# Kernel optimization log

Measured on AMD Instinct MI355X. Metric: run time of the kernel, lower is better.

## Reference

```python
import jax, jax.numpy as jnp
import numpy as np

B, C, L = 16, 512, 4096
G = 32
CPG = C // G          # 16
HALF = CPG // 2       # 8
EPS = 1e-5


def setup_inputs() -> dict:
    key = jax.random.key(0)
    k = jax.random.split(key, 5)
    return {
        "x": jax.random.normal(k[0], (B, C, L), dtype=jnp.float32),
        "cw_w": jax.random.normal(k[1], (G,), dtype=jnp.float32),
        "cw_b": jax.random.normal(k[2], (G,), dtype=jnp.float32),
        "sw_w": jax.random.normal(k[3], (G,), dtype=jnp.float32),
        "sw_b": jax.random.normal(k[4], (G,), dtype=jnp.float32),
        "gn_w": jnp.ones((G, HALF), dtype=jnp.float32),
        "gn_b": jnp.zeros((G, HALF), dtype=jnp.float32),
    }


def reference(x, cw_w, cw_b, sw_w, sw_b, gn_w, gn_b):
    b, c, l = x.shape
    g = cw_w.shape[0]
    cpg = c // g
    half = cpg // 2
    xg = x.reshape(b, g, cpg, l)
    x1 = xg[:, :, :half, :]   # [B,G,half,L] channel-attention half
    x2 = xg[:, :, half:, :]   # [B,G,half,L] spatial-attention half

    # channel attention: per-channel temporal mean -> scalar affine + sigmoid
    ca = x1.mean(axis=3)                                          # [B,G,half]
    w1 = jax.nn.sigmoid(ca * cw_w[None, :, None] + cw_b[None, :, None])
    x1e = x1 * w1[..., None]

    # GroupNorm(1, half): normalize over (channels, length) per (sample, group)
    mu = x2.mean(axis=(2, 3), keepdims=True)
    var = x2.var(axis=(2, 3), keepdims=True)                      # biased var, as in torch GroupNorm
    xn = (x2 - mu) * jax.lax.rsqrt(var + EPS)
    xn = xn * gn_w[None, :, :, None] + gn_b[None, :, :, None]

    # spatial attention: channel-mean of normalized -> scalar affine + sigmoid
    sm = xn.mean(axis=2)                                          # [B,G,L]
    w2 = jax.nn.sigmoid(sm * sw_w[None, :, None] + sw_b[None, :, None])
    x2e = x2 * w2[:, :, None, :]

    out = jnp.concatenate([x1e, x2e], axis=2)                     # [B,G,cpg,L]
    # final channel shuffle: view->transpose(1,2)->view
    out = out.transpose(0, 2, 1, 3).reshape(b, c, l)
    return out
```

## Files before the change

kernel.cpp:

```cpp
#include <hip/hip_runtime.h>
#include <math.h>

#define Bdim 16
#define Cdim 512
#define Ldim 4096
#define Gdim 32
#define CPG  16
#define HALF 8
#define EPSV 1e-5f

#define THREADS 512
#define NWAVES  (THREADS / 64)

__device__ __forceinline__ float wave_reduce_sum(float v) {
#pragma unroll
    for (int off = 32; off > 0; off >>= 1)
        v += __shfl_xor(v, off, 64);
    return v;
}

__device__ __forceinline__ float sigmoidf_(float x) {
    return 1.0f / (1.0f + expf(-x));
}

__global__ __launch_bounds__(THREADS, 4) void fused_ham_kernel(
    const float* __restrict__ x,
    const float* __restrict__ cw_w, const float* __restrict__ cw_b,
    const float* __restrict__ sw_w, const float* __restrict__ sw_b,
    const float* __restrict__ gn_w, const float* __restrict__ gn_b,
    float* __restrict__ out)
{
    const int bg   = blockIdx.x;
    const int b    = bg / Gdim;
    const int g    = bg % Gdim;
    const int tid  = threadIdx.x;
    const int wave = tid >> 6;
    const int lane = tid & 63;

    __shared__ float red1[NWAVES][HALF];
    __shared__ float red2[NWAVES][2];

    const float* xb   = x + ((size_t)b * Cdim + (size_t)g * CPG) * Ldim;
    float*       outb = out + (size_t)b * Cdim * Ldim;

    const int l0 = tid * 4;

    float4 a[HALF][2];
    float  s1[HALF];
#pragma unroll
    for (int c = 0; c < HALF; ++c) {
        s1[c] = 0.f;
#pragma unroll
        for (int j = 0; j < 2; ++j) {
            const float4 v = *reinterpret_cast<const float4*>(
                xb + (size_t)c * Ldim + j * (Ldim / 2) + l0);
            a[c][j] = v;
            s1[c] += (v.x + v.y) + (v.z + v.w);
        }
    }
#pragma unroll
    for (int c = 0; c < HALF; ++c) {
        const float t = wave_reduce_sum(s1[c]);
        if (lane == 0) red1[wave][c] = t;
    }
    __syncthreads();

    float w1[HALF];
    {
        const float cww = cw_w[g], cwb = cw_b[g];
#pragma unroll
        for (int c = 0; c < HALF; ++c) {
            float s = 0.f;
#pragma unroll
            for (int w = 0; w < NWAVES; ++w) s += red1[w][c];
            const float ca = s * (1.0f / Ldim);
            w1[c] = sigmoidf_(ca * cww + cwb);
        }
    }

#pragma unroll
    for (int c = 0; c < HALF; ++c) {
        float* o = outb + (size_t)(c * Gdim + g) * Ldim;
#pragma unroll
        for (int j = 0; j < 2; ++j) {
            float4 v = a[c][j];
            v.x *= w1[c]; v.y *= w1[c]; v.z *= w1[c]; v.w *= w1[c];
            *reinterpret_cast<float4*>(o + j * (Ldim / 2) + l0) = v;
        }
    }

    float4 bb[HALF][2];
    float  sum = 0.f, ssq = 0.f;
#pragma unroll
    for (int c = 0; c < HALF; ++c) {
#pragma unroll
        for (int j = 0; j < 2; ++j) {
            const float4 v = *reinterpret_cast<const float4*>(
                xb + (size_t)(HALF + c) * Ldim + j * (Ldim / 2) + l0);
            bb[c][j] = v;
            sum += (v.x + v.y) + (v.z + v.w);
            ssq += (v.x * v.x + v.y * v.y) + (v.z * v.z + v.w * v.w);
        }
    }
    sum = wave_reduce_sum(sum);
    ssq = wave_reduce_sum(ssq);
    if (lane == 0) { red2[wave][0] = sum; red2[wave][1] = ssq; }
    __syncthreads();

    float tsum = 0.f, tssq = 0.f;
#pragma unroll
    for (int w = 0; w < NWAVES; ++w) { tsum += red2[w][0]; tssq += red2[w][1]; }
    const float inv_n = 1.0f / (HALF * Ldim);
    const float mu    = tsum * inv_n;
    const float var   = tssq * inv_n - mu * mu;
    const float rs    = rsqrtf(var + EPSV);

    float gw[HALF];
    float sgw = 0.f, mgb = 0.f;
#pragma unroll
    for (int c = 0; c < HALF; ++c) {
        gw[c] = gn_w[g * HALF + c];
        sgw  += gw[c];
        mgb  += gn_b[g * HALF + c];
    }
    mgb *= (1.0f / HALF);
    const float sww = sw_w[g], swb = sw_b[g];

#pragma unroll
    for (int j = 0; j < 2; ++j) {
        float4 ws; ws.x = 0.f; ws.y = 0.f; ws.z = 0.f; ws.w = 0.f;
#pragma unroll
        for (int c = 0; c < HALF; ++c) {
            ws.x += gw[c] * bb[c][j].x;
            ws.y += gw[c] * bb[c][j].y;
            ws.z += gw[c] * bb[c][j].z;
            ws.w += gw[c] * bb[c][j].w;
        }
        const float k0 = rs * (1.0f / HALF);
        const float koff = -mu * sgw;
        float4 w2;
        w2.x = sigmoidf_(((ws.x + koff) * k0 + mgb) * sww + swb);
        w2.y = sigmoidf_(((ws.y + koff) * k0 + mgb) * sww + swb);
        w2.z = sigmoidf_(((ws.z + koff) * k0 + mgb) * sww + swb);
        w2.w = sigmoidf_(((ws.w + koff) * k0 + mgb) * sww + swb);

#pragma unroll
        for (int c = 0; c < HALF; ++c) {
            float* o = outb + (size_t)((HALF + c) * Gdim + g) * Ldim;
            float4 v = bb[c][j];
            v.x *= w2.x; v.y *= w2.y; v.z *= w2.z; v.w *= w2.w;
            *reinterpret_cast<float4*>(o + j * (Ldim / 2) + l0) = v;
        }
    }
}

extern "C" void kernel_launch(void* const* d_in, const int* in_sizes, int n_in,
                              void* d_out, int out_size, void* d_ws, size_t ws_size,
                              hipStream_t stream) {
    const float* x    = (const float*)d_in[0];
    const float* cw_w = (const float*)d_in[1];
    const float* cw_b = (const float*)d_in[2];
    const float* sw_w = (const float*)d_in[3];
    const float* sw_b = (const float*)d_in[4];
    const float* gn_w = (const float*)d_in[5];
    const float* gn_b = (const float*)d_in[6];
    float* out = (float*)d_out;

    fused_ham_kernel<<<dim3(Bdim * Gdim), dim3(THREADS), 0, stream>>>(
        x, cw_w, cw_b, sw_w, sw_b, gn_w, gn_b, out);
}
```

Before: 53.68 us.

## Split fused kernel into stats, finalize, and apply passes over L-slices

Replaces the single fused kernel, which ran one block per (batch, group) and held the whole group in registers, with three kernels. The first computes partial statistics over quarter-length slices, the second combines them into per-group coefficients, and the third re-reads x to apply the attention weights. This spreads the work over four times as many smaller blocks to raise occupancy and parallelism. The cost is a second full read of x from memory and two extra kernel launches.

```diff
diff --git a/kernel.cpp b/kernel.cpp
--- a/kernel.cpp
+++ b/kernel.cpp
@@ -9,8 +9,15 @@
 #define HALF 8
 #define EPSV 1e-5f
 
-#define THREADS 512
+#define THREADS 256
 #define NWAVES  (THREADS / 64)
+#define QSPLIT  4
+#define NBG     (Bdim * Gdim)
+#define NBLK    (NBG * QSPLIT)
+#define LSLICE  (Ldim / QSPLIT)
+
+#define WS_PART_STRIDE 10
+#define WS_STATS_OFF   (NBG * QSPLIT * WS_PART_STRIDE)
 
 __device__ __forceinline__ float wave_reduce_sum(float v) {
 #pragma unroll
@@ -23,134 +30,155 @@
     return 1.0f / (1.0f + expf(-x));
 }
 
-__global__ __launch_bounds__(THREADS, 4) void fused_ham_kernel(
-    const float* __restrict__ x,
+__global__ __launch_bounds__(THREADS, 8) void k1_stats(
+    const float* __restrict__ x, float* __restrict__ ws)
+{
+    const int bid = blockIdx.x;
+    const int bg  = bid >> 2;
+    const int q   = bid & 3;
+    const int b   = bg >> 5;
+    const int g   = bg & 31;
+    const int tid = threadIdx.x;
+    const int wave = tid >> 6;
+    const int lane = tid & 63;
+
+    const float* xb = x + ((size_t)b * Cdim + (size_t)g * CPG) * Ldim
+                        + q * LSLICE + tid * 4;
+
+    float acc[10];
+#pragma unroll
+    for (int k = 0; k < 10; ++k) acc[k] = 0.f;
+
+#pragma unroll
+    for (int c = 0; c < HALF; ++c) {
+        const float4 v = *reinterpret_cast<const float4*>(xb + (size_t)c * Ldim);
+        acc[c] = (v.x + v.y) + (v.z + v.w);
+    }
+#pragma unroll
+    for (int c = 0; c < HALF; ++c) {
+        const float4 v = *reinterpret_cast<const float4*>(xb + (size_t)(HALF + c) * Ldim);
+        acc[8] += (v.x + v.y) + (v.z + v.w);
+        acc[9] += (v.x * v.x + v.y * v.y) + (v.z * v.z + v.w * v.w);
+    }
+
+    __shared__ float red[NWAVES][10];
+#pragma unroll
+    for (int k = 0; k < 10; ++k) {
+        const float t = wave_reduce_sum(acc[k]);
+        if (lane == 0) red[wave][k] = t;
+    }
+    __syncthreads();
+
+    if (tid < 10) {
+        float s = 0.f;
+#pragma unroll
+        for (int w = 0; w < NWAVES; ++w) s += red[w][tid];
+        ws[(size_t)bid * WS_PART_STRIDE + tid] = s;
+    }
+}
+
+__global__ __launch_bounds__(THREADS) void k2_finalize(
+    const float* __restrict__ ws_in, float* __restrict__ ws_out,
     const float* __restrict__ cw_w, const float* __restrict__ cw_b,
     const float* __restrict__ sw_w, const float* __restrict__ sw_b,
-    const float* __restrict__ gn_w, const float* __restrict__ gn_b,
-    float* __restrict__ out)
+    const float* __restrict__ gn_w, const float* __restrict__ gn_b)
 {
-    const int bg   = blockIdx.x;
-    const int b    = bg / Gdim;
-    const int g    = bg % Gdim;
-    const int tid  = threadIdx.x;
-    const int wave = tid >> 6;
-    const int lane = tid & 63;
-
-    __shared__ float red1[NWAVES][HALF];
-    __shared__ float red2[NWAVES][2];
-
-    const float* xb   = x + ((size_t)b * Cdim + (size_t)g * CPG) * Ldim;
-    float*       outb = out + (size_t)b * Cdim * Ldim;
-
-    const int l0 = tid * 4;
-
-    float4 a[HALF][2];
-    float  s1[HALF];
-#pragma unroll
-    for (int c = 0; c < HALF; ++c) {
-        s1[c] = 0.f;
-#pragma unroll
-        for (int j = 0; j < 2; ++j) {
-            const float4 v = *reinterpret_cast<const float4*>(
-                xb + (size_t)c * Ldim + j * (Ldim / 2) + l0);
-            a[c][j] = v;
-            s1[c] += (v.x + v.y) + (v.z + v.w);
-        }
-    }
-#pragma unroll
-    for (int c = 0; c < HALF; ++c) {
-        const float t = wave_reduce_sum(s1[c]);
-        if (lane == 0) red1[wave][c] = t;
-    }
-    __syncthreads();
-
-    float w1[HALF];
-    {
-        const float cww = cw_w[g], cwb = cw_b[g];
-#pragma unroll
-        for (int c = 0; c < HALF; ++c) {
-            float s = 0.f;
-#pragma unroll
-            for (int w = 0; w < NWAVES; ++w) s += red1[w][c];
-            const float ca = s * (1.0f / Ldim);
-            w1[c] = sigmoidf_(ca * cww + cwb);
-        }
-    }
-
-#pragma unroll
-    for (int c = 0; c < HALF; ++c) {
-        float* o = outb + (size_t)(c * Gdim + g) * Ldim;
-#pragma unroll
-        for (int j = 0; j < 2; ++j) {
-            float4 v = a[c][j];
-            v.x *= w1[c]; v.y *= w1[c]; v.z *= w1[c]; v.w *= w1[c];
-            *reinterpret_cast<float4*>(o + j * (Ldim / 2) + l0) = v;
-        }
-    }
-
-    float4 bb[HALF][2];
-    float  sum = 0.f, ssq = 0.f;
-#pragma unroll
-    for (int c = 0; c < HALF; ++c) {
-#pragma unroll
-        for (int j = 0; j < 2; ++j) {
-            const float4 v = *reinterpret_cast<const float4*>(
-                xb + (size_t)(HALF + c) * Ldim + j * (Ldim / 2) + l0);
-            bb[c][j] = v;
-            sum += (v.x + v.y) + (v.z + v.w);
-            ssq += (v.x * v.x + v.y * v.y) + (v.z * v.z + v.w * v.w);
-        }
-    }
-    sum = wave_reduce_sum(sum);
-    ssq = wave_reduce_sum(ssq);
-    if (lane == 0) { red2[wave][0] = sum; red2[wave][1] = ssq; }
-    __syncthreads();
-
-    float tsum = 0.f, tssq = 0.f;
-#pragma unroll
-    for (int w = 0; w < NWAVES; ++w) { tsum += red2[w][0]; tssq += red2[w][1]; }
+    const int bg = blockIdx.x * THREADS + threadIdx.x;
+    if (bg >= NBG) return;
+    const int g = bg & 31;
+
+    float s[10];
+#pragma unroll
+    for (int k = 0; k < 10; ++k) {
+        float t = 0.f;
+#pragma unroll
+        for (int q = 0; q < QSPLIT; ++q)
+            t += ws_in[((size_t)bg * QSPLIT + q) * WS_PART_STRIDE + k];
+        s[k] = t;
+    }
+
+    const float cww = cw_w[g], cwb = cw_b[g];
+    float* o = ws_out + (size_t)bg * 10;
+#pragma unroll
+    for (int c = 0; c < HALF; ++c) {
+        const float ca = s[c] * (1.0f / Ldim);
+        o[c] = sigmoidf_(ca * cww + cwb);
+    }
+
     const float inv_n = 1.0f / (HALF * Ldim);
-    const float mu    = tsum * inv_n;
-    const float var   = tssq * inv_n - mu * mu;
-    const float rs    = rsqrtf(var + EPSV);
-
-    float gw[HALF];
+    const float mu  = s[8] * inv_n;
+    const float var = s[9] * inv_n - mu * mu;
+    const float rs  = rsqrtf(var + EPSV);
+
     float sgw = 0.f, mgb = 0.f;
 #pragma unroll
     for (int c = 0; c < HALF; ++c) {
-        gw[c] = gn_w[g * HALF + c];
-        sgw  += gw[c];
-        mgb  += gn_b[g * HALF + c];
+        sgw += gn_w[g * HALF + c];
+        mgb += gn_b[g * HALF + c];
     }
     mgb *= (1.0f / HALF);
+
     const float sww = sw_w[g], swb = sw_b[g];
-
-#pragma unroll
-    for (int j = 0; j < 2; ++j) {
-        float4 ws; ws.x = 0.f; ws.y = 0.f; ws.z = 0.f; ws.w = 0.f;
-#pragma unroll
-        for (int c = 0; c < HALF; ++c) {
-            ws.x += gw[c] * bb[c][j].x;
-            ws.y += gw[c] * bb[c][j].y;
-            ws.z += gw[c] * bb[c][j].z;
-            ws.w += gw[c] * bb[c][j].w;
-        }
-        const float k0 = rs * (1.0f / HALF);
-        const float koff = -mu * sgw;
-        float4 w2;
-        w2.x = sigmoidf_(((ws.x + koff) * k0 + mgb) * sww + swb);
-        w2.y = sigmoidf_(((ws.y + koff) * k0 + mgb) * sww + swb);
-        w2.z = sigmoidf_(((ws.z + koff) * k0 + mgb) * sww + swb);
-        w2.w = sigmoidf_(((ws.w + koff) * k0 + mgb) * sww + swb);
-
-#pragma unroll
-        for (int c = 0; c < HALF; ++c) {
-            float* o = outb + (size_t)((HALF + c) * Gdim + g) * Ldim;
-            float4 v = bb[c][j];
-            v.x *= w2.x; v.y *= w2.y; v.z *= w2.z; v.w *= w2.w;
-            *reinterpret_cast<float4*>(o + j * (Ldim / 2) + l0) = v;
-        }
+    const float k0  = rs * (1.0f / HALF);
+    o[8] = k0 * sww;
+    o[9] = (-mu * sgw * k0 + mgb) * sww + swb;
+}
+
+__global__ __launch_bounds__(THREADS, 8) void k3_apply(
+    const float* __restrict__ x, const float* __restrict__ stats,
+    const float* __restrict__ gn_w, float* __restrict__ out)
+{
+    const int bid = blockIdx.x;
+    const int bg  = bid >> 2;
+    const int q   = bid & 3;
+    const int b   = bg >> 5;
+    const int g   = bg & 31;
+    const int tid = threadIdx.x;
+
+    const size_t loff = (size_t)(q * LSLICE + tid * 4);
+    const float* xb   = x + ((size_t)b * Cdim + (size_t)g * CPG) * Ldim + loff;
+    float*       outb = out + (size_t)b * Cdim * Ldim + loff;
+
+    const float* st = stats + (size_t)bg * 10;
+    const float A2 = st[8], B2 = st[9];
+
+    float4 a[HALF];
+#pragma unroll
+    for (int c = 0; c < HALF; ++c)
+        a[c] = *reinterpret_cast<const float4*>(xb + (size_t)c * Ldim);
+#pragma unroll
+    for (int c = 0; c < HALF; ++c) {
+        const float w1 = st[c];
+        float4 v = a[c];
+        v.x *= w1; v.y *= w1; v.z *= w1; v.w *= w1;
+        *reinterpret_cast<float4*>(outb + (size_t)(c * Gdim + g) * Ldim) = v;
+    }
+
+    float4 bb[HALF];
+#pragma unroll
+    for (int c = 0; c < HALF; ++c)
+        bb[c] = *reinterpret_cast<const float4*>(xb + (size_t)(HALF + c) * Ldim);
+
+    float4 wsum; wsum.x = 0.f; wsum.y = 0.f; wsum.z = 0.f; wsum.w = 0.f;
+#pragma unroll
+    for (int c = 0; c < HALF; ++c) {
+        const float gw = gn_w[g * HALF + c];
+        wsum.x += gw * bb[c].x;
+        wsum.y += gw * bb[c].y;
+        wsum.z += gw * bb[c].z;
+        wsum.w += gw * bb[c].w;
+    }
+    float4 w2;
+    w2.x = sigmoidf_(A2 * wsum.x + B2);
+    w2.y = sigmoidf_(A2 * wsum.y + B2);
+    w2.z = sigmoidf_(A2 * wsum.z + B2);
+    w2.w = sigmoidf_(A2 * wsum.w + B2);
+
+#pragma unroll
+    for (int c = 0; c < HALF; ++c) {
+        float4 v = bb[c];
+        v.x *= w2.x; v.y *= w2.y; v.z *= w2.z; v.w *= w2.w;
+        *reinterpret_cast<float4*>(outb + (size_t)((HALF + c) * Gdim + g) * Ldim) = v;
     }
 }
 
@@ -165,7 +193,13 @@
     const float* gn_w = (const float*)d_in[5];
     const float* gn_b = (const float*)d_in[6];
     float* out = (float*)d_out;
-
-    fused_ham_kernel<<<dim3(Bdim * Gdim), dim3(THREADS), 0, stream>>>(
-        x, cw_w, cw_b, sw_w, sw_b, gn_w, gn_b, out);
-}
+    float* ws  = (float*)d_ws;
+
+    float* ws_part  = ws;
+    float* ws_stats = ws + WS_STATS_OFF;
+
+    k1_stats<<<dim3(NBLK), dim3(THREADS), 0, stream>>>(x, ws_part);
+    k2_finalize<<<dim3((NBG + THREADS - 1) / THREADS), dim3(THREADS), 0, stream>>>(
+        ws_part, ws_stats, cw_w, cw_b, sw_w, sw_b, gn_w, gn_b);
+    k3_apply<<<dim3(NBLK), dim3(THREADS), 0, stream>>>(x, ws_stats, gn_w, out);
+}
```

New measurement: 72.46 us. 1.35x slower.

## Split channel and spatial halves into separate blocks, re-read inputs instead of holding registers

Applied to the files above, without the earlier changes.

Launches twice as many blocks: one set handles the channel-attention half with one wave per channel row and no block-level sync, the other handles the GroupNorm/spatial half. Inputs are re-read from global memory (expected to hit cache) instead of being held in large register arrays, which lowers register pressure and allows the higher occupancy target in launch bounds. The spatial affine and sigmoid constants are folded into a single multiply-add. The cost is extra global or cache reads of x for the second pass.

```diff
diff --git a/kernel.cpp b/kernel.cpp
--- a/kernel.cpp
+++ b/kernel.cpp
@@ -11,6 +11,7 @@
 
 #define THREADS 512
 #define NWAVES  (THREADS / 64)
+#define NBG     (Bdim * Gdim)
 
 __device__ __forceinline__ float wave_reduce_sum(float v) {
 #pragma unroll
@@ -23,133 +24,110 @@
     return 1.0f / (1.0f + expf(-x));
 }
 
-__global__ __launch_bounds__(THREADS, 4) void fused_ham_kernel(
+__global__ __launch_bounds__(THREADS, 8) void fused_ham_kernel(
     const float* __restrict__ x,
     const float* __restrict__ cw_w, const float* __restrict__ cw_b,
     const float* __restrict__ sw_w, const float* __restrict__ sw_b,
     const float* __restrict__ gn_w, const float* __restrict__ gn_b,
     float* __restrict__ out)
 {
-    const int bg   = blockIdx.x;
-    const int b    = bg / Gdim;
-    const int g    = bg % Gdim;
+    const int bid  = blockIdx.x;
+    const int ph   = bid >> 9;
+    const int bg   = bid & (NBG - 1);
+    const int b    = bg >> 5;
+    const int g    = bg & 31;
     const int tid  = threadIdx.x;
     const int wave = tid >> 6;
     const int lane = tid & 63;
 
-    __shared__ float red1[NWAVES][HALF];
-    __shared__ float red2[NWAVES][2];
-
     const float* xb   = x + ((size_t)b * Cdim + (size_t)g * CPG) * Ldim;
     float*       outb = out + (size_t)b * Cdim * Ldim;
 
-    const int l0 = tid * 4;
+    if (ph == 0) {
+        const float* row = xb + (size_t)wave * Ldim;
+        float s = 0.f;
+#pragma unroll
+        for (int k = 0; k < 16; ++k) {
+            const float4 v = *reinterpret_cast<const float4*>(row + k * 256 + lane * 4);
+            s += (v.x + v.y) + (v.z + v.w);
+        }
+        s = wave_reduce_sum(s);
+        const float ca = s * (1.0f / Ldim);
+        const float w1 = sigmoidf_(ca * cw_w[g] + cw_b[g]);
 
-    float4 a[HALF][2];
-    float  s1[HALF];
+        float* orow = outb + (size_t)(wave * Gdim + g) * Ldim;
 #pragma unroll
-    for (int c = 0; c < HALF; ++c) {
-        s1[c] = 0.f;
+        for (int k = 0; k < 16; ++k) {
+            float4 v = *reinterpret_cast<const float4*>(row + k * 256 + lane * 4);
+            v.x *= w1; v.y *= w1; v.z *= w1; v.w *= w1;
+            *reinterpret_cast<float4*>(orow + k * 256 + lane * 4) = v;
+        }
+    } else {
+        const float* row = xb + (size_t)(HALF + wave) * Ldim;
+        float sum = 0.f, ssq = 0.f;
 #pragma unroll
-        for (int j = 0; j < 2; ++j) {
-            const float4 v = *reinterpret_cast<const float4*>(
-                xb + (size_t)c * Ldim + j * (Ldim / 2) + l0);
-            a[c][j] = v;
-            s1[c] += (v.x + v.y) + (v.z + v.w);
-        }
-    }
-#pragma unroll
-    for (int c = 0; c < HALF; ++c) {
-        const float t = wave_reduce_sum(s1[c]);
-        if (lane == 0) red1[wave][c] = t;
-    }
-    __syncthreads();
-
-    float w1[HALF];
-    {
-        const float cww = cw_w[g], cwb = cw_b[g];
-#pragma unroll
-        for (int c = 0; c < HALF; ++c) {
-            float s = 0.f;
-#pragma unroll
-            for (int w = 0; w < NWAVES; ++w) s += red1[w][c];
-            const float ca = s * (1.0f / Ldim);
-            w1[c] = sigmoidf_(ca * cww + cwb);
-        }
-    }
-
-#pragma unroll
-    for (int c = 0; c < HALF; ++c) {
-        float* o = outb + (size_t)(c * Gdim + g) * Ldim;
-#pragma unroll
-        for (int j = 0; j < 2; ++j) {
-            float4 v = a[c][j];
-            v.x *= w1[c]; v.y *= w1[c]; v.z *= w1[c]; v.w *= w1[c];
-            *reinterpret_cast<float4*>(o + j * (Ldim / 2) + l0) = v;
-        }
-    }
-
-    float4 bb[HALF][2];
-    float  sum = 0.f, ssq = 0.f;
-#pragma unroll
-    for (int c = 0; c < HALF; ++c) {
-#pragma unroll
-        for (int j = 0; j < 2; ++j) {
-            const float4 v = *reinterpret_cast<const float4*>(
-                xb + (size_t)(HALF + c) * Ldim + j * (Ldim / 2) + l0);
-            bb[c][j] = v;
+        for (int k = 0; k < 16; ++k) {
+            const float4 v = *reinterpret_cast<const float4*>(row + k * 256 + lane * 4);
             sum += (v.x + v.y) + (v.z + v.w);
             ssq += (v.x * v.x + v.y * v.y) + (v.z * v.z + v.w * v.w);
         }
-    }
-    sum = wave_reduce_sum(sum);
-    ssq = wave_reduce_sum(ssq);
-    if (lane == 0) { red2[wave][0] = sum; red2[wave][1] = ssq; }
-    __syncthreads();
+        sum = wave_reduce_sum(sum);
+        ssq = wave_reduce_sum(ssq);
 
-    float tsum = 0.f, tssq = 0.f;
+        __shared__ float red[NWAVES][2];
+        if (lane == 0) { red[wave][0] = sum; red[wave][1] = ssq; }
+        __syncthreads();
+
+        float tsum = 0.f, tssq = 0.f;
 #pragma unroll
-    for (int w = 0; w < NWAVES; ++w) { tsum += red2[w][0]; tssq += red2[w][1]; }
-    const float inv_n = 1.0f / (HALF * Ldim);
-    const float mu    = tsum * inv_n;
-    const float var   = tssq * inv_n - mu * mu;
-    const float rs    = rsqrtf(var + EPSV);
+        for (int w = 0; w < NWAVES; ++w) { tsum += red[w][0]; tssq += red[w][1]; }
+        const float inv_n = 1.0f / (HALF * Ldim);
+        const float mu  = tsum * inv_n;
+        const float var = tssq * inv_n - mu * mu;
+        const float rs  = rsqrtf(var + EPSV);
 
-    float gw[HALF];
-    float sgw = 0.f, mgb = 0.f;
+        float gw[HALF];
+        float sgw = 0.f, mgb = 0.f;
 #pragma unroll
-    for (int c = 0; c < HALF; ++c) {
-        gw[c] = gn_w[g * HALF + c];
-        sgw  += gw[c];
-        mgb  += gn_b[g * HALF + c];
-    }
-    mgb *= (1.0f / HALF);
-    const float sww = sw_w[g], swb = sw_b[g];
+        for (int c = 0; c < HALF; ++c) {
+            gw[c] = gn_w[g * HALF + c];
+            sgw  += gw[c];
+            mgb  += gn_b[g * HALF + c];
+        }
+        mgb *= (1.0f / HALF);
+        const float k0 = rs * (1.0f / HALF);
+        const float A2 = k0 * sw_w[g];
+        const float B2 = (-mu * sgw * k0 + mgb) * sw_w[g] + sw_b[g];
+
+        const float* xb2 = xb + (size_t)HALF * Ldim;
+#pragma unroll
+        for (int j = 0; j < 2; ++j) {
+            const int l0 = tid * 4 + j * (Ldim / 2);
+            float4 bb[HALF];
+#pragma unroll
+            for (int c = 0; c < HALF; ++c)
+                bb[c] = *reinterpret_cast<const float4*>(xb2 + (size_t)c * Ldim + l0);
+
+            float4 wsum; wsum.x = 0.f; wsum.y = 0.f; wsum.z = 0.f; wsum.w = 0.f;
+#pragma unroll
+            for (int c = 0; c < HALF; ++c) {
+                wsum.x += gw[c] * bb[c].x;
+                wsum.y += gw[c] * bb[c].y;
+                wsum.z += gw[c] * bb[c].z;
+                wsum.w += gw[c] * bb[c].w;
+            }
+            float4 w2;
+            w2.x = sigmoidf_(A2 * wsum.x + B2);
+            w2.y = sigmoidf_(A2 * wsum.y + B2);
+            w2.z = sigmoidf_(A2 * wsum.z + B2);
+            w2.w = sigmoidf_(A2 * wsum.w + B2);
 
 #pragma unroll
-    for (int j = 0; j < 2; ++j) {
-        float4 ws; ws.x = 0.f; ws.y = 0.f; ws.z = 0.f; ws.w = 0.f;
-#pragma unroll
-        for (int c = 0; c < HALF; ++c) {
-            ws.x += gw[c] * bb[c][j].x;
-            ws.y += gw[c] * bb[c][j].y;
-            ws.z += gw[c] * bb[c][j].z;
-            ws.w += gw[c] * bb[c][j].w;
-        }
-        const float k0 = rs * (1.0f / HALF);
-        const float koff = -mu * sgw;
-        float4 w2;
-        w2.x = sigmoidf_(((ws.x + koff) * k0 + mgb) * sww + swb);
-        w2.y = sigmoidf_(((ws.y + koff) * k0 + mgb) * sww + swb);
-        w2.z = sigmoidf_(((ws.z + koff) * k0 + mgb) * sww + swb);
-        w2.w = sigmoidf_(((ws.w + koff) * k0 + mgb) * sww + swb);
-
-#pragma unroll
-        for (int c = 0; c < HALF; ++c) {
-            float* o = outb + (size_t)((HALF + c) * Gdim + g) * Ldim;
-            float4 v = bb[c][j];
-            v.x *= w2.x; v.y *= w2.y; v.z *= w2.z; v.w *= w2.w;
-            *reinterpret_cast<float4*>(o + j * (Ldim / 2) + l0) = v;
+            for (int c = 0; c < HALF; ++c) {
+                float4 v = bb[c];
+                v.x *= w2.x; v.y *= w2.y; v.z *= w2.z; v.w *= w2.w;
+                *reinterpret_cast<float4*>(outb + (size_t)((HALF + c) * Gdim + g) * Ldim + l0) = v;
+            }
         }
     }
 }
@@ -166,6 +144,6 @@
     const float* gn_b = (const float*)d_in[6];
     float* out = (float*)d_out;
 
-    fused_ham_kernel<<<dim3(Bdim * Gdim), dim3(THREADS), 0, stream>>>(
+    fused_ham_kernel<<<dim3(2 * NBG), dim3(THREADS), 0, stream>>>(
         x, cw_w, cw_b, sw_w, sw_b, gn_w, gn_b, out);
 }
```

Measured after the change: 65.69 us. +22.4%, slower.
